# Kernel tuning notes

Hardware: AMD Instinct MI355X
Metric: run time of the kernel (lower is better)

## Reference

```python
import jax, jax.numpy as jnp
import numpy as np
import math

HASHMAP_SIZE = 1 << 17
N_LEVELS = 16
N_FEATURES = 2
BASE_RES = 16.0
GROWTH = 1.5  # per-level resolution growth factor
PRIME_Y = np.uint32(2654435761)  # Instant-NGP spatial hash prime


def hash_encode(x, encoding):
    """Multiresolution 2D hash-grid encoding with bilinear interpolation.
    x: [N, 2] in [0,1); encoding: [T, L, F]. Returns [N, L*F]."""
    N = x.shape[0]
    scales = jnp.asarray(BASE_RES * GROWTH ** np.arange(N_LEVELS),
                         dtype=x.dtype)  # [L]
    pos = x[:, None, :] * scales[None, :, None]        # [N, L, 2]
    pf = jnp.floor(pos)
    frac = pos - pf                                    # [N, L, 2]
    pi = pf.astype(jnp.uint32)                         # integer corner base
    lvl = jnp.arange(N_LEVELS)[None, :]                # [1, L]

    feat = jnp.zeros((N, N_LEVELS, N_FEATURES), dtype=x.dtype)
    for cx in (0, 1):
        for cy in (0, 1):
            ix = pi[..., 0] + jnp.uint32(cx)
            iy = pi[..., 1] + jnp.uint32(cy)
            h = ix ^ (iy * PRIME_Y)                    # spatial hash (wraps mod 2^32)
            idx = (h & jnp.uint32(HASHMAP_SIZE - 1)).astype(jnp.int32)  # [N, L]
            wx = frac[..., 0] if cx else 1.0 - frac[..., 0]
            wy = frac[..., 1] if cy else 1.0 - frac[..., 1]
            feat = feat + (wx * wy)[..., None] * encoding[idx, lvl]  # gather [N,L,F]
    return feat.reshape(N, N_LEVELS * N_FEATURES)


def setup_inputs() -> dict:
    key = jax.random.key(0)
    ks = jax.random.split(key, 8)
    N = 1 << 20
    n_neurons = [32, 64, 64, 3]
    x = jax.random.uniform(ks[0], (N, 2), dtype=jnp.float32)
    # encoding init: rand * 2e-4 - 1e-4
    encoding = jax.random.uniform(ks[1], (HASHMAP_SIZE, N_LEVELS, N_FEATURES),
                                  dtype=jnp.float32) * 2e-4 - 1e-4
    inp = {"x": x, "encoding": encoding}
    for i in range(3):
        s = 1.0 / math.sqrt(n_neurons[i])
        w = jax.random.uniform(ks[2 + i], (n_neurons[i], n_neurons[i + 1]),
                               dtype=jnp.float32) * 2 * s - s
        b = jax.random.uniform(ks[5 + i], (n_neurons[i + 1],),
                               dtype=jnp.float32) * 2 * s - s
        inp[f"w{i}"] = w
        inp[f"b{i}"] = b
    return inp


def reference(x, encoding, w0, b0, w1, b1, w2, b2):
    feat = hash_encode(x, encoding)                 # [N, 32]
    h = jax.nn.relu(feat @ w0 + b0)                 # [N, 64]
    h = jax.nn.relu(h @ w1 + b1)                    # [N, 64]
    return h @ w2 + b2                              # [N, 3]
```

## Files before the change

kernel.cpp:

```cpp
#include <hip/hip_runtime.h>
#include <stdint.h>

typedef __bf16 bf16_t;
typedef bf16_t bf16x8 __attribute__((ext_vector_type(8)));
typedef float  f32x4  __attribute__((ext_vector_type(4)));
typedef float  f32x2v __attribute__((ext_vector_type(2)));

static constexpr uint32_t PRIME = 2654435761u;
static constexpr uint32_t HMASK = (1u << 17) - 1u;
static constexpr uint32_t TSIZE = 1u << 17;

static constexpr int NLDS   = 5308;
static constexpr int NDALL  = 136642;

static constexpr float FSCALE = 8192.0f;
static constexpr float WSCALE = 1.0f / 8192.0f;

__device__ __forceinline__ uint32_t fbits(float f) {
    union { float f; uint32_t u; } v; v.f = f; return v.u;
}
__device__ __forceinline__ float asfloat(uint32_t u) {
    union { uint32_t u; float f; } v; v.u = u; return v.f;
}

__device__ __forceinline__ uint32_t enc8(float v) {
    const uint32_t s = (fbits(v) >> 24) & 0x80u;
    float m = fabsf(v) * 0x1p-120f;
    uint32_t u = fbits(m);
    u += 0x7FFFFu + ((u >> 20) & 1u);
    return s | ((u >> 20) & 0x7fu);
}
__device__ __forceinline__ uint32_t pack8(float a, float b) {
#if __has_builtin(__builtin_amdgcn_cvt_pk_fp8_f32)
    return (uint32_t)__builtin_amdgcn_cvt_pk_fp8_f32(a, b, 0, false) & 0xffffu;
#else
    return enc8(a) | (enc8(b) << 8);
#endif
}
__device__ __forceinline__ float2 unpack8(uint32_t u) {
#if __has_builtin(__builtin_amdgcn_cvt_pk_f32_fp8)
    f32x2v r = __builtin_amdgcn_cvt_pk_f32_fp8((int)u, false);
    return make_float2(r.x, r.y);
#else
    const float f0 = asfloat(((u & 0x80u) << 24) | ((u & 0x7fu) << 20)) * 0x1p120f;
    const float f1 = asfloat(((u & 0x8000u) << 16) | ((u & 0x7f00u) << 12)) * 0x1p120f;
    return make_float2(f0, f1);
#endif
}

__global__ __launch_bounds__(256)
void repack_enc8(const float2* __restrict__ src, uint16_t* __restrict__ dst) {
    __shared__ uint16_t ldsT[8 * 257];
    const int tid = threadIdx.x;
    const int t0  = blockIdx.x * 256;
#pragma unroll
    for (int k = 0; k < 8; ++k) {
        const int j = k * 256 + tid;
        const int tl = j >> 3, l8 = j & 7;
        const float2 f = src[((size_t)(t0 + tl) << 4) + 8 + l8];
        ldsT[l8 * 257 + tl] = (uint16_t)pack8(f.x * FSCALE, f.y * FSCALE);
    }
    __syncthreads();
#pragma unroll
    for (int k = 0; k < 8; ++k)
        dst[((uint32_t)k << 17) + t0 + tid] = ldsT[k * 257 + tid];
}

__global__ __launch_bounds__(256)
void densify_enc(const float2* __restrict__ src, uint16_t* __restrict__ dst) {
    const int i = blockIdx.x * 256 + threadIdx.x;
    if (i >= NDALL) return;
    int lvl, W, off;
    if      (i <   289) { lvl = 0; W =  17; off = 0;     }
    else if (i <   914) { lvl = 1; W =  25; off = 289;   }
    else if (i <  2283) { lvl = 2; W =  37; off = 914;   }
    else if (i <  5308) { lvl = 3; W =  55; off = 2283;  }
    else if (i < 12032) { lvl = 4; W =  82; off = 5308;  }
    else if (i < 27161) { lvl = 5; W = 123; off = 12032; }
    else if (i < 61017) { lvl = 6; W = 184; off = 27161; }
    else                { lvl = 7; W = 275; off = 61017; }
    const int li = i - off;
    const uint32_t iy = (uint32_t)(li / W), ix = (uint32_t)(li % W);
    const uint32_t h = (ix ^ (iy * PRIME)) & HMASK;
    const float2 f = src[h * 16 + lvl];
    dst[i] = (uint16_t)pack8(f.x * FSCALE, f.y * FSCALE);
}

__global__ __launch_bounds__(256, 2)
void fused_hash_mlp(const float* __restrict__ xin,
                    const uint16_t* __restrict__ tab8,
                    const uint16_t* __restrict__ dense,
                    const float* __restrict__ w0, const float* __restrict__ b0,
                    const float* __restrict__ w1, const float* __restrict__ b1,
                    const float* __restrict__ w2, const float* __restrict__ b2,
                    float* __restrict__ out,
                    int nGroups)
{
    __shared__ uint16_t ldsTab[NLDS];
    __shared__ __align__(16) bf16_t lds[4 * 16 * 80];

    const int tid  = threadIdx.x;
    const int wib  = tid >> 6;
    const int lane = tid & 63;
    const int q    = lane >> 4;
    const int n16  = lane & 15;

    bf16_t* myLds = &lds[wib * (16 * 80)];

    for (int i = tid; i < NLDS; i += 256) ldsTab[i] = dense[i];

    bf16x8 Bw0[4], Bw1[2][4], Bw2[2];
#pragma unroll
    for (int t = 0; t < 4; ++t)
#pragma unroll
        for (int j = 0; j < 8; ++j)
            Bw0[t][j] = (bf16_t)(w0[(q * 8 + j) * 64 + t * 16 + n16] * WSCALE);
#pragma unroll
    for (int c = 0; c < 2; ++c)
#pragma unroll
        for (int t = 0; t < 4; ++t)
#pragma unroll
            for (int j = 0; j < 8; ++j)
                Bw1[c][t][j] = (bf16_t)w1[(c * 32 + q * 8 + j) * 64 + t * 16 + n16];
#pragma unroll
    for (int c = 0; c < 2; ++c)
#pragma unroll
        for (int j = 0; j < 8; ++j)
            Bw2[c][j] = (n16 < 3) ? (bf16_t)w2[(c * 32 + q * 8 + j) * 3 + n16]
                                  : (bf16_t)0.0f;

    float bv0[4], bv1[4];
#pragma unroll
    for (int t = 0; t < 4; ++t) {
        bv0[t] = b0[t * 16 + n16];
        bv1[t] = b1[t * 16 + n16];
    }
    const float bv2 = (n16 < 3) ? b2[n16] : 0.0f;

    const float sb = 16.0f * ((q == 0) ? 1.0f :
                              (q == 1) ? 5.0625f :
                              (q == 2) ? 25.62890625f :
                                         129.746337890625f);
    const float sc[4] = { sb, sb * 1.5f, sb * 2.25f, sb * 3.375f };

    const uint32_t l8base = ((uint32_t)((q >= 2 ? q - 2 : 0) * 4)) << 17;

    __syncthreads();

    for (int g = blockIdx.x; g < nGroups; g += gridDim.x) {
        const int tile = g * 4 + wib;
        const int p = tile * 16 + n16;
        const float2 xy = ((const float2*)xin)[p];
        const float px = xy.x, py = xy.y;

        bf16x8 af;
#pragma unroll
        for (int lv = 0; lv < 4; ++lv) {
            const float posx = px * sc[lv], posy = py * sc[lv];
            const float fx = floorf(posx), fy = floorf(posy);
            const float frx = posx - fx,  fry = posy - fy;
            const uint32_t ix = (uint32_t)fx, iy = (uint32_t)fy;

            const uint32_t Wl = (lv == 0) ? 17u  : (lv == 1) ? 25u
                              : (lv == 2) ? 37u  : 55u;
            const uint32_t Ol = (lv == 0) ? 0u   : (lv == 1) ? 289u
                              : (lv == 2) ? 914u : 2283u;
            const uint32_t Wg = (lv == 0) ? 82u    : (lv == 1) ? 123u
                              : (lv == 2) ? 184u   : 275u;
            const uint32_t Og = (lv == 0) ? 5308u  : (lv == 1) ? 12032u
                              : (lv == 2) ? 27161u : 61017u;

            uint32_t u00, u10, u01, u11;
            if (q == 0) {
                const uint32_t a = Ol + iy * Wl + ix;
                u00 = ldsTab[a];
                u10 = ldsTab[a + 1];
                u01 = ldsTab[a + Wl];
                u11 = ldsTab[a + Wl + 1];
            } else if (q == 1) {
                const uint32_t a = Og + iy * Wg + ix;
                u00 = dense[a];
                u10 = dense[a + 1];
                u01 = dense[a + Wg];
                u11 = dense[a + Wg + 1];
            } else {
                const uint32_t hy0 = iy * PRIME, hy1 = hy0 + PRIME;
                const uint32_t i00 = ( ix       ^ hy0) & HMASK;
                const uint32_t i10 = ((ix + 1u) ^ hy0) & HMASK;
                const uint32_t i01 = ( ix       ^ hy1) & HMASK;
                const uint32_t i11 = ((ix + 1u) ^ hy1) & HMASK;
                const uint32_t base = l8base + ((uint32_t)lv << 17);
                u00 = tab8[base + i00];
                u10 = tab8[base + i10];
                u01 = tab8[base + i01];
                u11 = tab8[base + i11];
            }

            const float2 e00 = unpack8(u00);
            const float2 e10 = unpack8(u10);
            const float2 e01 = unpack8(u01);
            const float2 e11 = unpack8(u11);
            const float wx1 = frx, wx0 = 1.0f - frx, wy1 = fry, wy0 = 1.0f - fry;
            const float w00 = wx0 * wy0, w10 = wx1 * wy0, w01 = wx0 * wy1, w11 = wx1 * wy1;
            const float f0 = w00 * e00.x + w10 * e10.x + w01 * e01.x + w11 * e11.x;
            const float f1 = w00 * e00.y + w10 * e10.y + w01 * e01.y + w11 * e11.y;
            af[2 * lv]     = (bf16_t)f0;
            af[2 * lv + 1] = (bf16_t)f1;
        }

        f32x4 c0[4];
#pragma unroll
        for (int t = 0; t < 4; ++t) {
            f32x4 cc = { bv0[t], bv0[t], bv0[t], bv0[t] };
            c0[t] = __builtin_amdgcn_mfma_f32_16x16x32_bf16(af, Bw0[t], cc, 0, 0, 0);
        }

#pragma unroll
        for (int t = 0; t < 4; ++t)
#pragma unroll
            for (int r = 0; r < 4; ++r)
                myLds[(q * 4 + r) * 80 + t * 16 + n16] = (bf16_t)fmaxf(c0[t][r], 0.0f);

        bf16x8 A1[2];
#pragma unroll
        for (int c = 0; c < 2; ++c)
            A1[c] = *(const bf16x8*)&myLds[n16 * 80 + c * 32 + q * 8];

        f32x4 c1[4];
#pragma unroll
        for (int t = 0; t < 4; ++t) {
            f32x4 cc = { bv1[t], bv1[t], bv1[t], bv1[t] };
            cc    = __builtin_amdgcn_mfma_f32_16x16x32_bf16(A1[0], Bw1[0][t], cc, 0, 0, 0);
            c1[t] = __builtin_amdgcn_mfma_f32_16x16x32_bf16(A1[1], Bw1[1][t], cc, 0, 0, 0);
        }

#pragma unroll
        for (int t = 0; t < 4; ++t)
#pragma unroll
            for (int r = 0; r < 4; ++r)
                myLds[(q * 4 + r) * 80 + t * 16 + n16] = (bf16_t)fmaxf(c1[t][r], 0.0f);

        bf16x8 A2[2];
#pragma unroll
        for (int c = 0; c < 2; ++c)
            A2[c] = *(const bf16x8*)&myLds[n16 * 80 + c * 32 + q * 8];

        f32x4 co = { bv2, bv2, bv2, bv2 };
        co = __builtin_amdgcn_mfma_f32_16x16x32_bf16(A2[0], Bw2[0], co, 0, 0, 0);
        co = __builtin_amdgcn_mfma_f32_16x16x32_bf16(A2[1], Bw2[1], co, 0, 0, 0);

        if (n16 < 3) {
#pragma unroll
            for (int r = 0; r < 4; ++r)
                out[(size_t)(tile * 16 + q * 4 + r) * 3 + n16] = co[r];
        }
    }
}

__global__ __launch_bounds__(256)
void fused_hash_mlp_fp32(const float* __restrict__ xin,
                         const float* __restrict__ enc,
                         const float* __restrict__ w0, const float* __restrict__ b0,
                         const float* __restrict__ w1, const float* __restrict__ b1,
                         const float* __restrict__ w2, const float* __restrict__ b2,
                         float* __restrict__ out,
                         int nGroups)
{
    __shared__ __align__(16) bf16_t lds[4 * 16 * 80];
    const int tid  = threadIdx.x;
    const int wib  = tid >> 6;
    const int lane = tid & 63;
    const int q    = lane >> 4;
    const int n16  = lane & 15;
    bf16_t* myLds = &lds[wib * (16 * 80)];

    bf16x8 Bw0[4], Bw1[2][4], Bw2[2];
#pragma unroll
    for (int t = 0; t < 4; ++t)
#pragma unroll
        for (int j = 0; j < 8; ++j)
            Bw0[t][j] = (bf16_t)w0[(q * 8 + j) * 64 + t * 16 + n16];
#pragma unroll
    for (int c = 0; c < 2; ++c)
#pragma unroll
        for (int t = 0; t < 4; ++t)
#pragma unroll
            for (int j = 0; j < 8; ++j)
                Bw1[c][t][j] = (bf16_t)w1[(c * 32 + q * 8 + j) * 64 + t * 16 + n16];
#pragma unroll
    for (int c = 0; c < 2; ++c)
#pragma unroll
        for (int j = 0; j < 8; ++j)
            Bw2[c][j] = (n16 < 3) ? (bf16_t)w2[(c * 32 + q * 8 + j) * 3 + n16]
                                  : (bf16_t)0.0f;

    float bv0[4], bv1[4];
#pragma unroll
    for (int t = 0; t < 4; ++t) { bv0[t] = b0[t * 16 + n16]; bv1[t] = b1[t * 16 + n16]; }
    const float bv2 = (n16 < 3) ? b2[n16] : 0.0f;

    const float sb = 16.0f * ((q == 0) ? 1.0f : (q == 1) ? 5.0625f :
                              (q == 2) ? 25.62890625f : 129.746337890625f);
    const float sc[4] = { sb, sb * 1.5f, sb * 2.25f, sb * 3.375f };
    const char* encB = (const char*)enc;
    const uint32_t lvBase = (uint32_t)q * 32u;

    for (int g = blockIdx.x; g < nGroups; g += gridDim.x) {
        const int tile = g * 4 + wib;
        const int p = tile * 16 + n16;
        const float2 xy = ((const float2*)xin)[p];
        const float px = xy.x, py = xy.y;

        bf16x8 af;
#pragma unroll
        for (int lv = 0; lv < 4; ++lv) {
            const float posx = px * sc[lv], posy = py * sc[lv];
            const float fx = floorf(posx), fy = floorf(posy);
            const float frx = posx - fx,  fry = posy - fy;
            const uint32_t ix = (uint32_t)fx, iy = (uint32_t)fy;
            const uint32_t hy0 = iy * PRIME, hy1 = hy0 + PRIME;
            const uint32_t i00 = ( ix       ^ hy0) & HMASK;
            const uint32_t i10 = ((ix + 1u) ^ hy0) & HMASK;
            const uint32_t i01 = ( ix       ^ hy1) & HMASK;
            const uint32_t i11 = ((ix + 1u) ^ hy1) & HMASK;
            const uint32_t off = lvBase + (uint32_t)lv * 8u;
            const float2 e00 = *(const float2*)(encB + (i00 * 128u + off));
            const float2 e10 = *(const float2*)(encB + (i10 * 128u + off));
            const float2 e01 = *(const float2*)(encB + (i01 * 128u + off));
            const float2 e11 = *(const float2*)(encB + (i11 * 128u + off));
            const float wx1 = frx, wx0 = 1.0f - frx, wy1 = fry, wy0 = 1.0f - fry;
            const float w00 = wx0 * wy0, w10 = wx1 * wy0, w01 = wx0 * wy1, w11 = wx1 * wy1;
            af[2 * lv]     = (bf16_t)(w00 * e00.x + w10 * e10.x + w01 * e01.x + w11 * e11.x);
            af[2 * lv + 1] = (bf16_t)(w00 * e00.y + w10 * e10.y + w01 * e01.y + w11 * e11.y);
        }

        f32x4 c0[4];
#pragma unroll
        for (int t = 0; t < 4; ++t) {
            f32x4 cc = { bv0[t], bv0[t], bv0[t], bv0[t] };
            c0[t] = __builtin_amdgcn_mfma_f32_16x16x32_bf16(af, Bw0[t], cc, 0, 0, 0);
        }
        __syncthreads();
#pragma unroll
        for (int t = 0; t < 4; ++t)
#pragma unroll
            for (int r = 0; r < 4; ++r)
                myLds[(q * 4 + r) * 80 + t * 16 + n16] = (bf16_t)fmaxf(c0[t][r], 0.0f);
        __syncthreads();
        bf16x8 A1[2];
#pragma unroll
        for (int c = 0; c < 2; ++c)
            A1[c] = *(const bf16x8*)&myLds[n16 * 80 + c * 32 + q * 8];

        f32x4 c1[4];
#pragma unroll
        for (int t = 0; t < 4; ++t) {
            f32x4 cc = { bv1[t], bv1[t], bv1[t], bv1[t] };
            cc    = __builtin_amdgcn_mfma_f32_16x16x32_bf16(A1[0], Bw1[0][t], cc, 0, 0, 0);
            c1[t] = __builtin_amdgcn_mfma_f32_16x16x32_bf16(A1[1], Bw1[1][t], cc, 0, 0, 0);
        }
        __syncthreads();
#pragma unroll
        for (int t = 0; t < 4; ++t)
#pragma unroll
            for (int r = 0; r < 4; ++r)
                myLds[(q * 4 + r) * 80 + t * 16 + n16] = (bf16_t)fmaxf(c1[t][r], 0.0f);
        __syncthreads();
        bf16x8 A2[2];
#pragma unroll
        for (int c = 0; c < 2; ++c)
            A2[c] = *(const bf16x8*)&myLds[n16 * 80 + c * 32 + q * 8];

        f32x4 co = { bv2, bv2, bv2, bv2 };
        co = __builtin_amdgcn_mfma_f32_16x16x32_bf16(A2[0], Bw2[0], co, 0, 0, 0);
        co = __builtin_amdgcn_mfma_f32_16x16x32_bf16(A2[1], Bw2[1], co, 0, 0, 0);
        if (n16 < 3) {
#pragma unroll
            for (int r = 0; r < 4; ++r)
                out[(size_t)(tile * 16 + q * 4 + r) * 3 + n16] = co[r];
        }
    }
}

extern "C" void kernel_launch(void* const* d_in, const int* in_sizes, int n_in,
                              void* d_out, int out_size, void* d_ws, size_t ws_size,
                              hipStream_t stream) {
    const float* x  = (const float*)d_in[0];
    const float* en = (const float*)d_in[1];
    const float* w0 = (const float*)d_in[2];
    const float* b0 = (const float*)d_in[3];
    const float* w1 = (const float*)d_in[4];
    const float* b1 = (const float*)d_in[5];
    const float* w2 = (const float*)d_in[6];
    const float* b2 = (const float*)d_in[7];
    float* out = (float*)d_out;

    const int N = in_sizes[0] / 2;
    const int nTiles = N / 16;
    const int nGroups = nTiles / 4;

    const size_t wsNeeded = ((size_t)TSIZE * 8 + NDALL) * 2;
    if (ws_size >= wsNeeded) {
        uint16_t* tab8  = (uint16_t*)d_ws;
        uint16_t* dense = tab8 + ((size_t)TSIZE * 8);
        repack_enc8<<<TSIZE / 256, 256, 0, stream>>>((const float2*)en, tab8);
        densify_enc<<<(NDALL + 255) / 256, 256, 0, stream>>>((const float2*)en, dense);
        int blocks = 2048;
        if (blocks > nGroups) blocks = nGroups;
        fused_hash_mlp<<<blocks, 256, 0, stream>>>(x, tab8, dense,
                                                   w0, b0, w1, b1, w2, b2, out, nGroups);
    } else {
        int blocks = 2048;
        if (blocks > nGroups) blocks = nGroups;
        fused_hash_mlp_fp32<<<blocks, 256, 0, stream>>>(x, en, w0, b0, w1, b1, w2, b2, out, nGroups);
    }
}
```

Baseline: 201.5 us.

## Pair adjacent x-corner table entries into 32-bit words to halve gathers

Adds a pre-pass that packs each dense-grid entry with its right neighbour into a 32-bit word, so the LDS and dense-global paths fetch two corners per load instead of one. For the hashed levels, it exploits the fact that ix^h and (ix+1)^h share a 32-bit word when ix is even, loading one word and issuing an extra 16-bit gather only for odd ix. This cuts the number of gather instructions at the cost of one more small preprocessing launch, doubled LDS footprint for the dense table, and divergent extra loads for odd ix.

Result: slower. 233.0 us (+15.6%).

```diff
diff --git a/kernel.cpp b/kernel.cpp
--- a/kernel.cpp
+++ b/kernel.cpp
@@ -86,18 +86,29 @@
     dst[i] = (uint16_t)pack8(f.x * FSCALE, f.y * FSCALE);
 }
 
+__global__ __launch_bounds__(256)
+void pairify_enc(const uint16_t* __restrict__ d16, uint32_t* __restrict__ dst) {
+    const int i = blockIdx.x * 256 + threadIdx.x;
+    if (i >= NDALL) return;
+    const uint32_t a = d16[i];
+    const uint32_t b = (i + 1 < NDALL) ? d16[i + 1] : 0u;
+    dst[i] = a | (b << 16);
+}
+
 __global__ __launch_bounds__(256, 2)
 void fused_hash_mlp(const float* __restrict__ xin,
-                    const uint16_t* __restrict__ tab8,
-                    const uint16_t* __restrict__ dense,
+                    const uint16_t* __restrict__ tab16,
+                    const uint32_t* __restrict__ dpair,
                     const float* __restrict__ w0, const float* __restrict__ b0,
                     const float* __restrict__ w1, const float* __restrict__ b1,
                     const float* __restrict__ w2, const float* __restrict__ b2,
                     float* __restrict__ out,
                     int nGroups)
 {
-    __shared__ uint16_t ldsTab[NLDS];
+    __shared__ uint32_t ldsTab[NLDS];
     __shared__ __align__(16) bf16_t lds[4 * 16 * 80];
+
+    const uint32_t* tab32 = (const uint32_t*)tab16;
 
     const int tid  = threadIdx.x;
     const int wib  = tid >> 6;
@@ -107,7 +118,7 @@
 
     bf16_t* myLds = &lds[wib * (16 * 80)];
 
-    for (int i = tid; i < NLDS; i += 256) ldsTab[i] = dense[i];
+    for (int i = tid; i < NLDS; i += 256) ldsTab[i] = dpair[i];
 
     bf16x8 Bw0[4], Bw1[2][4], Bw2[2];
 #pragma unroll
@@ -172,28 +183,48 @@
 
             uint32_t u00, u10, u01, u11;
             if (q == 0) {
-                const uint32_t a = Ol + iy * Wl + ix;
-                u00 = ldsTab[a];
-                u10 = ldsTab[a + 1];
-                u01 = ldsTab[a + Wl];
-                u11 = ldsTab[a + Wl + 1];
+                const uint32_t a  = Ol + iy * Wl + ix;
+                const uint32_t p0 = ldsTab[a];
+                const uint32_t p1 = ldsTab[a + Wl];
+                u00 = p0 & 0xffffu; u10 = p0 >> 16;
+                u01 = p1 & 0xffffu; u11 = p1 >> 16;
             } else if (q == 1) {
-                const uint32_t a = Og + iy * Wg + ix;
-                u00 = dense[a];
-                u10 = dense[a + 1];
-                u01 = dense[a + Wg];
-                u11 = dense[a + Wg + 1];
+                const uint32_t a  = Og + iy * Wg + ix;
+                const uint32_t p0 = dpair[a];
+                const uint32_t p1 = dpair[a + Wg];
+                u00 = p0 & 0xffffu; u10 = p0 >> 16;
+                u01 = p1 & 0xffffu; u11 = p1 >> 16;
             } else {
                 const uint32_t hy0 = iy * PRIME, hy1 = hy0 + PRIME;
-                const uint32_t i00 = ( ix       ^ hy0) & HMASK;
-                const uint32_t i10 = ((ix + 1u) ^ hy0) & HMASK;
-                const uint32_t i01 = ( ix       ^ hy1) & HMASK;
-                const uint32_t i11 = ((ix + 1u) ^ hy1) & HMASK;
                 const uint32_t base = l8base + ((uint32_t)lv << 17);
-                u00 = tab8[base + i00];
-                u10 = tab8[base + i10];
-                u01 = tab8[base + i01];
-                u11 = tab8[base + i11];
+                const uint32_t iex = ix & ~1u;
+                const uint32_t odd = ix & 1u;
+                {
+                    const uint32_t ie = (iex ^ hy0) & HMASK;
+                    const uint32_t pr = tab32[(base >> 1) + (ie >> 1)];
+                    const uint32_t lo = pr & 0xffffu, hi = pr >> 16;
+                    const uint32_t uA = (ie & 1u) ? hi : lo;
+                    const uint32_t uB = (ie & 1u) ? lo : hi;
+                    u00 = odd ? uB : uA;
+                    u10 = uB;
+                    if (odd) {
+                        const uint32_t io = ((ix + 1u) ^ hy0) & HMASK;
+                        u10 = tab16[base + io];
+                    }
+                }
+                {
+                    const uint32_t ie = (iex ^ hy1) & HMASK;
+                    const uint32_t pr = tab32[(base >> 1) + (ie >> 1)];
+                    const uint32_t lo = pr & 0xffffu, hi = pr >> 16;
+                    const uint32_t uA = (ie & 1u) ? hi : lo;
+                    const uint32_t uB = (ie & 1u) ? lo : hi;
+                    u01 = odd ? uB : uA;
+                    u11 = uB;
+                    if (odd) {
+                        const uint32_t io = ((ix + 1u) ^ hy1) & HMASK;
+                        u11 = tab16[base + io];
+                    }
+                }
             }
 
             const float2 e00 = unpack8(u00);
@@ -399,15 +430,17 @@
     const int nTiles = N / 16;
     const int nGroups = nTiles / 4;
 
-    const size_t wsNeeded = ((size_t)TSIZE * 8 + NDALL) * 2;
+    const size_t wsNeeded = (size_t)TSIZE * 8 * 2 + (size_t)NDALL * 4 + (size_t)NDALL * 2;
     if (ws_size >= wsNeeded) {
         uint16_t* tab8  = (uint16_t*)d_ws;
-        uint16_t* dense = tab8 + ((size_t)TSIZE * 8);
+        uint32_t* dpair = (uint32_t*)(tab8 + (size_t)TSIZE * 8);
+        uint16_t* d16   = (uint16_t*)(dpair + NDALL);
         repack_enc8<<<TSIZE / 256, 256, 0, stream>>>((const float2*)en, tab8);
-        densify_enc<<<(NDALL + 255) / 256, 256, 0, stream>>>((const float2*)en, dense);
+        densify_enc<<<(NDALL + 255) / 256, 256, 0, stream>>>((const float2*)en, d16);
+        pairify_enc<<<(NDALL + 255) / 256, 256, 0, stream>>>(d16, dpair);
         int blocks = 2048;
         if (blocks > nGroups) blocks = nGroups;
-        fused_hash_mlp<<<blocks, 256, 0, stream>>>(x, tab8, dense,
+        fused_hash_mlp<<<blocks, 256, 0, stream>>>(x, tab8, dpair,
                                                    w0, b0, w1, b1, w2, b2, out, nGroups);
     } else {
         int blocks = 2048;
```

## Software-pipeline hash gathers one tile ahead and raise occupancy target

Applied to the files above, without the earlier changes.

Splits the loop body into a gather phase and a compute phase and issues the next tile's table loads, plus the coordinates for the tile after that, before running the MLP on the current tile. The goal is to hide global and LDS gather latency behind the MFMA work. Launch bounds also change from 2 to 4 blocks per SM, which caps registers per thread. The prefetched gathers hold extra registers, so that cap may cause spills. Near the end of the grid stride, the prefetch repeats the last valid group instead of reading out of bounds.

New measurement: 363.3 us. +80.3%, slower.

```diff
diff --git a/kernel.cpp b/kernel.cpp
--- a/kernel.cpp
+++ b/kernel.cpp
@@ -86,7 +86,7 @@
     dst[i] = (uint16_t)pack8(f.x * FSCALE, f.y * FSCALE);
 }
 
-__global__ __launch_bounds__(256, 2)
+__global__ __launch_bounds__(256, 4)
 void fused_hash_mlp(const float* __restrict__ xin,
                     const uint16_t* __restrict__ tab8,
                     const uint16_t* __restrict__ dense,
@@ -147,20 +147,19 @@
 
     __syncthreads();
 
-    for (int g = blockIdx.x; g < nGroups; g += gridDim.x) {
+    const int stride = gridDim.x;
+
+    auto loadXY = [&](int g) -> float2 {
         const int tile = g * 4 + wib;
-        const int p = tile * 16 + n16;
-        const float2 xy = ((const float2*)xin)[p];
-        const float px = xy.x, py = xy.y;
-
-        bf16x8 af;
+        return ((const float2*)xin)[tile * 16 + n16];
+    };
+
+    auto gather = [&](const float2 xy, uint32_t (&u)[4][4]) {
 #pragma unroll
         for (int lv = 0; lv < 4; ++lv) {
-            const float posx = px * sc[lv], posy = py * sc[lv];
-            const float fx = floorf(posx), fy = floorf(posy);
-            const float frx = posx - fx,  fry = posy - fy;
-            const uint32_t ix = (uint32_t)fx, iy = (uint32_t)fy;
-
+            const float posx = xy.x * sc[lv], posy = xy.y * sc[lv];
+            const uint32_t ix = (uint32_t)floorf(posx);
+            const uint32_t iy = (uint32_t)floorf(posy);
             const uint32_t Wl = (lv == 0) ? 17u  : (lv == 1) ? 25u
                               : (lv == 2) ? 37u  : 55u;
             const uint32_t Ol = (lv == 0) ? 0u   : (lv == 1) ? 289u
@@ -169,43 +168,44 @@
                               : (lv == 2) ? 184u   : 275u;
             const uint32_t Og = (lv == 0) ? 5308u  : (lv == 1) ? 12032u
                               : (lv == 2) ? 27161u : 61017u;
-
-            uint32_t u00, u10, u01, u11;
             if (q == 0) {
                 const uint32_t a = Ol + iy * Wl + ix;
-                u00 = ldsTab[a];
-                u10 = ldsTab[a + 1];
-                u01 = ldsTab[a + Wl];
-                u11 = ldsTab[a + Wl + 1];
+                u[lv][0] = ldsTab[a];
+                u[lv][1] = ldsTab[a + 1];
+                u[lv][2] = ldsTab[a + Wl];
+                u[lv][3] = ldsTab[a + Wl + 1];
             } else if (q == 1) {
                 const uint32_t a = Og + iy * Wg + ix;
-                u00 = dense[a];
-                u10 = dense[a + 1];
-                u01 = dense[a + Wg];
-                u11 = dense[a + Wg + 1];
+                u[lv][0] = dense[a];
+                u[lv][1] = dense[a + 1];
+                u[lv][2] = dense[a + Wg];
+                u[lv][3] = dense[a + Wg + 1];
             } else {
                 const uint32_t hy0 = iy * PRIME, hy1 = hy0 + PRIME;
-                const uint32_t i00 = ( ix       ^ hy0) & HMASK;
-                const uint32_t i10 = ((ix + 1u) ^ hy0) & HMASK;
-                const uint32_t i01 = ( ix       ^ hy1) & HMASK;
-                const uint32_t i11 = ((ix + 1u) ^ hy1) & HMASK;
                 const uint32_t base = l8base + ((uint32_t)lv << 17);
-                u00 = tab8[base + i00];
-                u10 = tab8[base + i10];
-                u01 = tab8[base + i01];
-                u11 = tab8[base + i11];
+                u[lv][0] = tab8[base + (( ix       ^ hy0) & HMASK)];
+                u[lv][1] = tab8[base + (((ix + 1u) ^ hy0) & HMASK)];
+                u[lv][2] = tab8[base + (( ix       ^ hy1) & HMASK)];
+                u[lv][3] = tab8[base + (((ix + 1u) ^ hy1) & HMASK)];
             }
-
-            const float2 e00 = unpack8(u00);
-            const float2 e10 = unpack8(u10);
-            const float2 e01 = unpack8(u01);
-            const float2 e11 = unpack8(u11);
+        }
+    };
+
+    auto processTile = [&](int g, const float2 xy, const uint32_t (&u)[4][4]) {
+        bf16x8 af;
+#pragma unroll
+        for (int lv = 0; lv < 4; ++lv) {
+            const float posx = xy.x * sc[lv], posy = xy.y * sc[lv];
+            const float frx = posx - floorf(posx);
+            const float fry = posy - floorf(posy);
+            const float2 e00 = unpack8(u[lv][0]);
+            const float2 e10 = unpack8(u[lv][1]);
+            const float2 e01 = unpack8(u[lv][2]);
+            const float2 e11 = unpack8(u[lv][3]);
             const float wx1 = frx, wx0 = 1.0f - frx, wy1 = fry, wy0 = 1.0f - fry;
             const float w00 = wx0 * wy0, w10 = wx1 * wy0, w01 = wx0 * wy1, w11 = wx1 * wy1;
-            const float f0 = w00 * e00.x + w10 * e10.x + w01 * e01.x + w11 * e11.x;
-            const float f1 = w00 * e00.y + w10 * e10.y + w01 * e01.y + w11 * e11.y;
-            af[2 * lv]     = (bf16_t)f0;
-            af[2 * lv + 1] = (bf16_t)f1;
+            af[2 * lv]     = (bf16_t)(w00 * e00.x + w10 * e10.x + w01 * e01.x + w11 * e11.x);
+            af[2 * lv + 1] = (bf16_t)(w00 * e00.y + w10 * e10.y + w01 * e01.y + w11 * e11.y);
         }
 
         f32x4 c0[4];
@@ -249,11 +249,37 @@
         co = __builtin_amdgcn_mfma_f32_16x16x32_bf16(A2[0], Bw2[0], co, 0, 0, 0);
         co = __builtin_amdgcn_mfma_f32_16x16x32_bf16(A2[1], Bw2[1], co, 0, 0, 0);
 
+        const int tile = g * 4 + wib;
         if (n16 < 3) {
 #pragma unroll
             for (int r = 0; r < 4; ++r)
                 out[(size_t)(tile * 16 + q * 4 + r) * 3 + n16] = co[r];
         }
+    };
+
+    int gA = blockIdx.x;
+    if (gA >= nGroups) return;
+    float2 xyA = loadXY(gA);
+    uint32_t u[4][4];
+    gather(xyA, u);
+    int gB = gA + stride; if (gB >= nGroups) gB = gA;
+    float2 xyB = loadXY(gB);
+
+    while (gA < nGroups) {
+        uint32_t un[4][4];
+        gather(xyB, un);
+        int gC = gB + stride; if (gC >= nGroups) gC = gB;
+        float2 xyC = loadXY(gC);
+
+        processTile(gA, xyA, u);
+
+        gA += stride;
+        xyA = xyB; xyB = xyC; gB = gC;
+#pragma unroll
+        for (int a = 0; a < 4; ++a)
+#pragma unroll
+            for (int b = 0; b < 4; ++b)
+                u[a][b] = un[a][b];
     }
 }
 
```
